# Kernel optimization log

Hardware: AMD Instinct MI355X
Metric: run time of the kernel (lower is better)

## Reference

```python
import jax, jax.numpy as jnp
import numpy as np
from jax import lax

T = 50
THETA = 1.0 - 0.0001  # max_1 - 0.0001, max_1 = T_win/T = 1.0


def conv_t(x, w, b, pad_h):
    # x: [N, C, H, W, T]; slayer conv3d has time-kernel 1 -> conv2d per timestep.
    n, c, h, wd, t = x.shape
    xb = jnp.moveaxis(x, -1, 1).reshape(n * t, c, h, wd)
    y = lax.conv_general_dilated(xb, w, (1, 1), [(pad_h, pad_h), (0, 0)])
    y = y + b[None, :, None, None]
    o, h2, w2 = y.shape[1], y.shape[2], y.shape[3]
    return jnp.moveaxis(y.reshape(n, t, o, h2, w2), 1, -1)


def if_spikes(a):
    # catCuda.getSpikes on an input stacked T times: IF neuron with constant
    # drive a per step, soft reset (v -= theta on spike). a: [N,C,H,W].
    def step(v, _):
        v = v + a
        s = (v >= THETA).astype(a.dtype)
        return v - s * THETA, s
    _, sp = lax.scan(step, jnp.zeros_like(a), None, length=T)
    return jnp.moveaxis(sp, 0, -1)  # [N,C,H,W,T]


def setup_inputs() -> dict:
    key = jax.random.key(0)
    ks = jax.random.split(key, 6)
    def w(k, shape, scale):
        return jax.random.normal(k, shape, jnp.float32) * scale
    x = jax.random.uniform(ks[0], (256, 1, 180, 1, T), jnp.float32)
    return {
        'x': x,
        'w1': w(ks[1], (16, 1, 3, 1), 0.3), 'b1': jnp.zeros(16, jnp.float32),
        'w2': w(ks[2], (32, 16, 9, 1), 0.1), 'b2': jnp.zeros(32, jnp.float32),
        'w3': w(ks[3], (32, 32, 7, 1), 0.1), 'b3': jnp.zeros(32, jnp.float32),
        'wf': w(ks[4], (4, 32, 83, 1), 0.05), 'bf': jnp.zeros(4, jnp.float32),
    }


def reference(x, w1, b1, w2, b2, w3, b3, wf, bf):
    y = conv_t(x, w1, b1, 1)                        # [N,16,180,1,T]
    y = if_spikes(jnp.sum(y, axis=4) / T)           # rate -> spikes
    y = conv_t(y, w2, b2, 1)                        # [N,32,174,1,T]
    y = if_spikes(jnp.sum(y, axis=4) / T)
    y = 1.1 * (y[:, :, 0::2] + y[:, :, 1::2])       # slayer sum-pool (2,1), weight 1.1
    y = if_spikes(jnp.sum(y, axis=4) / T)           # [N,32,87,1,T]
    y = conv_t(y, w3, b3, 1)                        # [N,32,83,1,T]
    y = if_spikes(jnp.sum(y, axis=4) / T)
    out = jnp.einsum('nchwt,ochw->not', y, wf) + bf[None, :, None]  # dense over full spatial
    return jnp.sum(out, axis=-1) / T                # sum_spikes / T -> [N,4]
```

## Files before the change

kernel.cpp:

```cpp
#include <hip/hip_runtime.h>


#define T_STEPS 50
#define THETA   0.9999f

#define F4C(v, c) ((c) == 0 ? (v).x : (c) == 1 ? (v).y : (c) == 2 ? (v).z : (v).w)

__device__ __forceinline__ float spike_rate(float a, const float* __restrict__ tbl) {
    constexpr float INV = 50.0f / 0.9999f;
    float t = a * INV;
    float c = fminf(fmaxf(floorf(t), 0.0f), 50.0f);
    bool risky = (t > 0.5f) && (fabsf(t - rintf(t)) < 2e-4f);
    if (__ballot(risky)) {
        float v = 0.f, cnt = 0.f;
#pragma unroll 1
        for (int k = 0; k < T_STEPS; ++k) {
            v += a;
            float s = (v >= THETA) ? 1.0f : 0.0f;
            v -= s * THETA;
            cnt += s;
        }
        c = cnt;
    }
    return tbl[(int)c];
}

__device__ __forceinline__ float spike_rate_nb(float a, const float* __restrict__ tbl) {
    constexpr float INV = 50.0f / 0.9999f;
    float t = a * INV;
    float c = fminf(fmaxf(floorf(t), 0.0f), 50.0f);
    return tbl[(int)c];
}

extern "C" __global__ void __launch_bounds__(1024, 4)
catnet_kernel(const float* __restrict__ x,
              const float* __restrict__ w1, const float* __restrict__ b1,
              const float* __restrict__ w2, const float* __restrict__ b2,
              const float* __restrict__ w3, const float* __restrict__ b3,
              const float* __restrict__ wf, const float* __restrict__ bf,
              float* __restrict__ out)
{
    const int n    = blockIdx.x;
    const int tid  = threadIdx.x;
    const int wave = tid >> 6;
    const int lane = tid & 63;

    __shared__ float  xbar[182];
    __shared__ float4 r1qe[4][92];
    __shared__ float4 r1qo[4][92];
    __shared__ float4 r3q[8][89];
    __shared__ alignas(16) float r4s[32][83];
    __shared__ float  ratetbl[51];
    __shared__ float  part[16];

    const float4 z4 = make_float4(0.f, 0.f, 0.f, 0.f);
    if (tid < 4)               r1qe[tid][0]       = z4;
    if (tid >= 4  && tid < 8)  r1qo[tid - 4][90]  = z4;
    if (tid >= 8  && tid < 16) r3q[tid - 8][0]    = z4;
    if (tid >= 16 && tid < 24) r3q[tid - 16][88]  = z4;
    if (tid == 64)             { xbar[0] = 0.f; xbar[181] = 0.f; }
    if (tid >= 128 && tid < 179) ratetbl[tid - 128] = (float)(tid - 128) / 50.0f;

    const float* xn = x + (size_t)n * (180 * 50);
    if (tid < 720) {
        const int h = tid >> 2, q = tid & 3;
        const float2* row2 = reinterpret_cast<const float2*>(xn + h * 50);
        float s = 0.f;
        for (int k = q; k < 24; k += 4) { float2 v = row2[k]; s += v.x + v.y; }
        if (q == 0)                     { float2 v = row2[24]; s += v.x + v.y; }
        s += __shfl_xor(s, 1, 4);
        s += __shfl_xor(s, 2, 4);
        if (q == 0) xbar[h + 1] = s;
    }
    __syncthreads();

    for (int idx = tid; idx < 16 * 180; idx += 1024) {
        int c = idx / 180, h = idx - c * 180;
        float a = w1[c*3+0] * xbar[h] + w1[c*3+1] * xbar[h+1] + w1[c*3+2] * xbar[h+2];
        a = a / 50.0f + b1[c];
        float r = spike_rate(a, ratetbl);
        int H = h + 1;
        float* dst = (H & 1) ? (float*)&r1qo[c >> 2][H >> 1]
                             : (float*)&r1qe[c >> 2][H >> 1];
        dst[c & 3] = r;
    }
    __syncthreads();

    {
        const int g   = __builtin_amdgcn_readfirstlane(tid >> 7);
        const int p   = tid & 127;
        const bool act = p < 87;
        const int pr  = act ? p : 0;
        const float* wb = w2 + g * 4 * 144;

        float a0[4], a1[4];
#pragma unroll
        for (int j = 0; j < 4; ++j) { a0[j] = b2[g*4 + j]; a1[j] = a0[j]; }

#pragma unroll 1
        for (int qd = 0; qd < 4; ++qd) {
            float4 we[5], wo[5];
#pragma unroll
            for (int d = 0; d < 5; ++d) { we[d] = r1qe[qd][pr + d]; wo[d] = r1qo[qd][pr + d]; }

#pragma unroll
            for (int c4 = 0; c4 < 4; ++c4) {
                const int ci = qd * 4 + c4;
#pragma unroll
                for (int j = 0; j < 4; ++j) {
                    const float* wj = wb + j * 144 + ci * 9;
#pragma unroll
                    for (int kh = 0; kh < 9; ++kh) {
                        float wv  = wj[kh];
                        float xlo = (kh & 1) ? F4C(wo[kh >> 1], c4)
                                             : F4C(we[kh >> 1], c4);
                        float xhi = (kh & 1) ? F4C(we[(kh + 1) >> 1], c4)
                                             : F4C(wo[kh >> 1], c4);
                        a0[j] += wv * xlo;
                        a1[j] += wv * xhi;
                    }
                }
            }
        }
        float r3t[4];
#pragma unroll
        for (int j = 0; j < 4; ++j) {
            float r20 = spike_rate(a0[j], ratetbl);
            float r21 = spike_rate(a1[j], ratetbl);
            r3t[j] = spike_rate_nb(1.1f * (r20 + r21), ratetbl);
        }
        if (act) r3q[g][p + 1] = make_float4(r3t[0], r3t[1], r3t[2], r3t[3]);
    }
    __syncthreads();

    {
        const int gg   = __builtin_amdgcn_readfirstlane(wave >> 1);
        const int g4   = gg * 4;
        const int half = wave & 1;
        const int cnt  = half ? 41 : 42;
        const bool act = lane < cnt;
        const int h0   = half * 42 + lane;
        const int hr   = act ? h0 : 0;
        const float* wb = w3 + g4 * 224;

        float a[4];
#pragma unroll
        for (int j = 0; j < 4; ++j) a[j] = b3[g4 + j];

#pragma unroll 1
        for (int q = 0; q < 8; ++q) {
            float4 rv[7];
#pragma unroll
            for (int d = 0; d < 7; ++d) rv[d] = r3q[q][hr + d];

#pragma unroll
            for (int c4 = 0; c4 < 4; ++c4) {
                const int ci = q * 4 + c4;
#pragma unroll
                for (int j = 0; j < 4; ++j) {
                    const float* wj = wb + j * 224 + ci * 7;
#pragma unroll
                    for (int kh = 0; kh < 7; ++kh)
                        a[j] += wj[kh] * F4C(rv[kh], c4);
                }
            }
        }
#pragma unroll
        for (int j = 0; j < 4; ++j) {
            float r = spike_rate(a[j], ratetbl);
            if (act) r4s[g4 + j][h0] = r;
        }
    }
    __syncthreads();

    {
        const int o = wave >> 2, q = wave & 3;
        const float2* r42 = reinterpret_cast<const float2*>(&r4s[0][0]);
        const float2* wo2 = reinterpret_cast<const float2*>(wf + o * (32 * 83));
        float acc = 0.f;
        for (int j = q * 64 + lane; j < 1328; j += 256) {
            float2 rv = r42[j], wv = wo2[j];
            acc += rv.x * wv.x + rv.y * wv.y;
        }
#pragma unroll
        for (int off = 32; off > 0; off >>= 1)
            acc += __shfl_down(acc, off, 64);
        if (lane == 0) part[wave] = acc;
    }
    __syncthreads();
    if (tid < 4) {
        float s = part[tid*4] + part[tid*4+1] + part[tid*4+2] + part[tid*4+3];
        out[n * 4 + tid] = s + bf[tid];
    }
}

extern "C" void kernel_launch(void* const* d_in, const int* in_sizes, int n_in,
                              void* d_out, int out_size, void* d_ws, size_t ws_size,
                              hipStream_t stream) {
    const float* x  = (const float*)d_in[0];
    const float* w1 = (const float*)d_in[1];
    const float* b1 = (const float*)d_in[2];
    const float* w2 = (const float*)d_in[3];
    const float* b2 = (const float*)d_in[4];
    const float* w3 = (const float*)d_in[5];
    const float* b3 = (const float*)d_in[6];
    const float* wf = (const float*)d_in[7];
    const float* bf = (const float*)d_in[8];
    float* outp = (float*)d_out;

    catnet_kernel<<<dim3(256), dim3(1024), 0, stream>>>(
        x, w1, b1, w2, b2, w3, b3, wf, bf, outp);
}
```

Before: 99.15 us.

## Split each sample across four blocks by spatial quarter with halo recompute

Each sample is now processed by four 512-thread blocks that each own a quarter of the output spatial positions. Each block recomputes the halo rows it needs from the earlier layers. Partial dense-layer sums go to a global buffer, and a second small kernel reduces them and adds the bias. The aim is to fill the GPU better than 256 blocks can (1024 blocks, higher occupancy), at the cost of redundant halo work and an extra kernel launch.

```diff
diff --git a/kernel.cpp b/kernel.cpp
--- a/kernel.cpp
+++ b/kernel.cpp
@@ -3,6 +3,8 @@
 
 #define T_STEPS 50
 #define THETA   0.9999f
+
+__device__ float g_part[256 * 16];
 
 #define F4C(v, c) ((c) == 0 ? (v).x : (c) == 1 ? (v).y : (c) == 2 ? (v).z : (v).w)
 
@@ -32,18 +34,27 @@
     return tbl[(int)c];
 }
 
-extern "C" __global__ void __launch_bounds__(1024, 4)
-catnet_kernel(const float* __restrict__ x,
-              const float* __restrict__ w1, const float* __restrict__ b1,
-              const float* __restrict__ w2, const float* __restrict__ b2,
-              const float* __restrict__ w3, const float* __restrict__ b3,
-              const float* __restrict__ wf, const float* __restrict__ bf,
-              float* __restrict__ out)
+extern "C" __global__ void __launch_bounds__(512, 8)
+catnet_split(const float* __restrict__ x,
+             const float* __restrict__ w1, const float* __restrict__ b1,
+             const float* __restrict__ w2, const float* __restrict__ b2,
+             const float* __restrict__ w3, const float* __restrict__ b3,
+             const float* __restrict__ wf)
 {
-    const int n    = blockIdx.x;
+    const int n    = blockIdx.x >> 2;
+    const int qt   = blockIdx.x & 3;
     const int tid  = threadIdx.x;
     const int wave = tid >> 6;
     const int lane = tid & 63;
+
+    const int h_lo_t[4]  = {0, 21, 42, 63},  h_cnt_t[4]  = {21, 21, 21, 20};
+    const int p_lo_t[4]  = {0, 20, 41, 62},  p_cnt_t[4]  = {27, 28, 28, 25};
+    const int r1_lo_t[4] = {0, 39, 81, 123}, r1_cnt_t[4] = {62, 65, 65, 57};
+    const int x_lo_t[4]  = {0, 38, 80, 122}, x_cnt_t[4]  = {63, 67, 67, 58};
+    const int h_lo  = h_lo_t[qt],  h_cnt  = h_cnt_t[qt];
+    const int p_lo  = p_lo_t[qt],  p_cnt  = p_cnt_t[qt];
+    const int r1_lo = r1_lo_t[qt], r1_cnt = r1_cnt_t[qt];
+    const int x_lo  = x_lo_t[qt],  x_cnt  = x_cnt_t[qt];
 
     __shared__ float  xbar[182];
     __shared__ float4 r1qe[4][92];
@@ -51,7 +62,7 @@
     __shared__ float4 r3q[8][89];
     __shared__ alignas(16) float r4s[32][83];
     __shared__ float  ratetbl[51];
-    __shared__ float  part[16];
+    __shared__ float  part[8];
 
     const float4 z4 = make_float4(0.f, 0.f, 0.f, 0.f);
     if (tid < 4)               r1qe[tid][0]       = z4;
@@ -62,8 +73,9 @@
     if (tid >= 128 && tid < 179) ratetbl[tid - 128] = (float)(tid - 128) / 50.0f;
 
     const float* xn = x + (size_t)n * (180 * 50);
-    if (tid < 720) {
-        const int h = tid >> 2, q = tid & 3;
+    if (tid < 4 * x_cnt) {
+        const int h_l = tid >> 2, q = tid & 3;
+        const int h   = x_lo + h_l;
         const float2* row2 = reinterpret_cast<const float2*>(xn + h * 50);
         float s = 0.f;
         for (int k = q; k < 24; k += 4) { float2 v = row2[k]; s += v.x + v.y; }
@@ -74,113 +86,113 @@
     }
     __syncthreads();
 
-    for (int idx = tid; idx < 16 * 180; idx += 1024) {
-        int c = idx / 180, h = idx - c * 180;
+    for (int idx = tid; idx < 16 * 128; idx += 512) {
+        const int c = idx >> 7, h_l = idx & 127;
+        const bool act = h_l < r1_cnt;
+        const int h = r1_lo + (act ? h_l : 0);
         float a = w1[c*3+0] * xbar[h] + w1[c*3+1] * xbar[h+1] + w1[c*3+2] * xbar[h+2];
         a = a / 50.0f + b1[c];
         float r = spike_rate(a, ratetbl);
-        int H = h + 1;
-        float* dst = (H & 1) ? (float*)&r1qo[c >> 2][H >> 1]
-                             : (float*)&r1qe[c >> 2][H >> 1];
-        dst[c & 3] = r;
+        if (act) {
+            int H = h + 1;
+            float* dst = (H & 1) ? (float*)&r1qo[c >> 2][H >> 1]
+                                 : (float*)&r1qe[c >> 2][H >> 1];
+            dst[c & 3] = r;
+        }
     }
     __syncthreads();
 
     {
-        const int g   = __builtin_amdgcn_readfirstlane(tid >> 7);
-        const int p   = tid & 127;
-        const bool act = p < 87;
-        const int pr  = act ? p : 0;
-        const float* wb = w2 + g * 4 * 144;
-
-        float a0[4], a1[4];
-#pragma unroll
-        for (int j = 0; j < 4; ++j) { a0[j] = b2[g*4 + j]; a1[j] = a0[j]; }
+        const int g   = __builtin_amdgcn_readfirstlane(wave);
+        if (lane < p_cnt) {
+            const int p = p_lo + lane;
+            const float* wb = w2 + g * 4 * 144;
+
+            float a0[4], a1[4];
+#pragma unroll
+            for (int j = 0; j < 4; ++j) { a0[j] = b2[g*4 + j]; a1[j] = a0[j]; }
 
 #pragma unroll 1
-        for (int qd = 0; qd < 4; ++qd) {
-            float4 we[5], wo[5];
-#pragma unroll
-            for (int d = 0; d < 5; ++d) { we[d] = r1qe[qd][pr + d]; wo[d] = r1qo[qd][pr + d]; }
-
-#pragma unroll
-            for (int c4 = 0; c4 < 4; ++c4) {
-                const int ci = qd * 4 + c4;
-#pragma unroll
-                for (int j = 0; j < 4; ++j) {
-                    const float* wj = wb + j * 144 + ci * 9;
-#pragma unroll
-                    for (int kh = 0; kh < 9; ++kh) {
-                        float wv  = wj[kh];
-                        float xlo = (kh & 1) ? F4C(wo[kh >> 1], c4)
-                                             : F4C(we[kh >> 1], c4);
-                        float xhi = (kh & 1) ? F4C(we[(kh + 1) >> 1], c4)
-                                             : F4C(wo[kh >> 1], c4);
-                        a0[j] += wv * xlo;
-                        a1[j] += wv * xhi;
+            for (int qd = 0; qd < 4; ++qd) {
+                float4 we[5], wo[5];
+#pragma unroll
+                for (int d = 0; d < 5; ++d) { we[d] = r1qe[qd][p + d]; wo[d] = r1qo[qd][p + d]; }
+
+#pragma unroll
+                for (int c4 = 0; c4 < 4; ++c4) {
+                    const int ci = qd * 4 + c4;
+#pragma unroll
+                    for (int j = 0; j < 4; ++j) {
+                        const float* wj = wb + j * 144 + ci * 9;
+#pragma unroll
+                        for (int kh = 0; kh < 9; ++kh) {
+                            float wv  = wj[kh];
+                            float xlo = (kh & 1) ? F4C(wo[kh >> 1], c4)
+                                                 : F4C(we[kh >> 1], c4);
+                            float xhi = (kh & 1) ? F4C(we[(kh + 1) >> 1], c4)
+                                                 : F4C(wo[kh >> 1], c4);
+                            a0[j] += wv * xlo;
+                            a1[j] += wv * xhi;
+                        }
                     }
                 }
             }
-        }
-        float r3t[4];
-#pragma unroll
-        for (int j = 0; j < 4; ++j) {
-            float r20 = spike_rate(a0[j], ratetbl);
-            float r21 = spike_rate(a1[j], ratetbl);
-            r3t[j] = spike_rate_nb(1.1f * (r20 + r21), ratetbl);
-        }
-        if (act) r3q[g][p + 1] = make_float4(r3t[0], r3t[1], r3t[2], r3t[3]);
+            float r3t[4];
+#pragma unroll
+            for (int j = 0; j < 4; ++j) {
+                float r20 = spike_rate(a0[j], ratetbl);
+                float r21 = spike_rate(a1[j], ratetbl);
+                r3t[j] = spike_rate_nb(1.1f * (r20 + r21), ratetbl);
+            }
+            r3q[g][p + 1] = make_float4(r3t[0], r3t[1], r3t[2], r3t[3]);
+        }
     }
     __syncthreads();
 
     {
-        const int gg   = __builtin_amdgcn_readfirstlane(wave >> 1);
-        const int g4   = gg * 4;
-        const int half = wave & 1;
-        const int cnt  = half ? 41 : 42;
-        const bool act = lane < cnt;
-        const int h0   = half * 42 + lane;
-        const int hr   = act ? h0 : 0;
-        const float* wb = w3 + g4 * 224;
-
-        float a[4];
-#pragma unroll
-        for (int j = 0; j < 4; ++j) a[j] = b3[g4 + j];
+        const int gg = __builtin_amdgcn_readfirstlane(wave);
+        const int g4 = gg * 4;
+        if (lane < h_cnt) {
+            const int h0 = h_lo + lane;
+            const float* wb = w3 + g4 * 224;
+
+            float a[4];
+#pragma unroll
+            for (int j = 0; j < 4; ++j) a[j] = b3[g4 + j];
 
 #pragma unroll 1
-        for (int q = 0; q < 8; ++q) {
-            float4 rv[7];
-#pragma unroll
-            for (int d = 0; d < 7; ++d) rv[d] = r3q[q][hr + d];
-
-#pragma unroll
-            for (int c4 = 0; c4 < 4; ++c4) {
-                const int ci = q * 4 + c4;
-#pragma unroll
-                for (int j = 0; j < 4; ++j) {
-                    const float* wj = wb + j * 224 + ci * 7;
-#pragma unroll
-                    for (int kh = 0; kh < 7; ++kh)
-                        a[j] += wj[kh] * F4C(rv[kh], c4);
+            for (int q = 0; q < 8; ++q) {
+                float4 rv[7];
+#pragma unroll
+                for (int d = 0; d < 7; ++d) rv[d] = r3q[q][h0 + d];
+
+#pragma unroll
+                for (int c4 = 0; c4 < 4; ++c4) {
+                    const int ci = q * 4 + c4;
+#pragma unroll
+                    for (int j = 0; j < 4; ++j) {
+                        const float* wj = wb + j * 224 + ci * 7;
+#pragma unroll
+                        for (int kh = 0; kh < 7; ++kh)
+                            a[j] += wj[kh] * F4C(rv[kh], c4);
+                    }
                 }
             }
-        }
-#pragma unroll
-        for (int j = 0; j < 4; ++j) {
-            float r = spike_rate(a[j], ratetbl);
-            if (act) r4s[g4 + j][h0] = r;
+#pragma unroll
+            for (int j = 0; j < 4; ++j)
+                r4s[g4 + j][h0] = spike_rate(a[j], ratetbl);
         }
     }
     __syncthreads();
 
     {
-        const int o = wave >> 2, q = wave & 3;
-        const float2* r42 = reinterpret_cast<const float2*>(&r4s[0][0]);
-        const float2* wo2 = reinterpret_cast<const float2*>(wf + o * (32 * 83));
+        const int o = wave >> 1, q = wave & 1;
         float acc = 0.f;
-        for (int j = q * 64 + lane; j < 1328; j += 256) {
-            float2 rv = r42[j], wv = wo2[j];
-            acc += rv.x * wv.x + rv.y * wv.y;
+        if (lane < h_cnt) {
+            const int h0 = h_lo + lane;
+            const float* wo = wf + o * (32 * 83);
+            for (int c = q; c < 32; c += 2)
+                acc += r4s[c][h0] * wo[c * 83 + h0];
         }
 #pragma unroll
         for (int off = 32; off > 0; off >>= 1)
@@ -188,9 +200,18 @@
         if (lane == 0) part[wave] = acc;
     }
     __syncthreads();
-    if (tid < 4) {
-        float s = part[tid*4] + part[tid*4+1] + part[tid*4+2] + part[tid*4+3];
-        out[n * 4 + tid] = s + bf[tid];
+    if (tid < 4)
+        g_part[n * 16 + qt * 4 + tid] = part[2 * tid] + part[2 * tid + 1];
+}
+
+extern "C" __global__ void __launch_bounds__(256)
+catnet_finish(const float* __restrict__ bf, float* __restrict__ out)
+{
+    const int i = blockIdx.x * 256 + threadIdx.x;
+    if (i < 1024) {
+        const int n = i >> 2, o = i & 3;
+        out[i] = g_part[n * 16 + o]     + g_part[n * 16 + 4 + o]
+               + g_part[n * 16 + 8 + o] + g_part[n * 16 + 12 + o] + bf[o];
     }
 }
 
@@ -208,6 +229,7 @@
     const float* bf = (const float*)d_in[8];
     float* outp = (float*)d_out;
 
-    catnet_kernel<<<dim3(256), dim3(1024), 0, stream>>>(
-        x, w1, b1, w2, b2, w3, b3, wf, bf, outp);
-}
+    catnet_split<<<dim3(1024), dim3(512), 0, stream>>>(
+        x, w1, b1, w2, b2, w3, b3, wf);
+    catnet_finish<<<dim3(4), dim3(256), 0, stream>>>(bf, outp);
+}
```

Result: slower. 110.0 us (+10.9%).
